# Kernel tuning notes

Hardware: AMD Instinct MI355X
Metric: run time of the kernel (lower is better)

## Reference

```python
import jax, jax.numpy as jnp
import numpy as np

FP8_E4M3_MAX = 448.0
AMAX_EPS = 1e-12


def _mlp(x, W1, b1, W2, b2):
    # wrapped sub-module: standard FFN block, exact (erf) GELU like nn.GELU
    h = jax.nn.gelu(x @ W1 + b1, approximate=False)  # [B,S,F]
    return h @ W2 + b2                               # [B,S,D]


def _quantize(t):
    # FP8ActivationStorage.quantize, simulated (int16) path:
    # amax -> scale = 448/amax -> scale*clamp -> cast int16 (truncates toward zero)
    amax = jnp.maximum(jnp.max(jnp.abs(t)), AMAX_EPS)
    scale = (FP8_E4M3_MAX / amax).astype(jnp.float32)
    q = jnp.clip(t.astype(jnp.float32) * scale, -FP8_E4M3_MAX, FP8_E4M3_MAX).astype(jnp.int16)
    return q, scale


def setup_inputs() -> dict:
    key = jax.random.key(0)
    k0, k1, k2 = jax.random.split(key, 3)
    B, S, D, F = 4, 4096, 2048, 8192
    x = jax.random.normal(k0, (B, S, D), dtype=jnp.float32)
    W1 = jax.random.normal(k1, (D, F), dtype=jnp.float32) * (1.0 / np.sqrt(D))
    b1 = jnp.zeros((F,), dtype=jnp.float32)
    W2 = jax.random.normal(k2, (F, D), dtype=jnp.float32) * (1.0 / np.sqrt(F))
    b2 = jnp.zeros((D,), dtype=jnp.float32)
    return {"x": x, "W1": W1, "b1": b1, "W2": W2, "b2": b2}


def reference(x, W1, b1, W2, b2):
    # Forward of _FP8CheckpointWrapper: run module on the ORIGINAL input,
    # and also compute the quantized copy that would be saved for backward.
    out = _mlp(x, W1, b1, W2, b2)
    q, scale = _quantize(jax.lax.stop_gradient(x))
    return out, q, scale
```

## Files before the change

### kernel.cpp

```cpp
#include <hip/hip_runtime.h>
#include <hip/hip_bf16.h>
#include <stdint.h>

#define BS_M 16384
#define DD   2048
#define FF   8192

typedef __attribute__((ext_vector_type(8))) short bf16x8;
typedef __attribute__((ext_vector_type(4))) float f32x4;

__device__ __forceinline__ void load_lds16(const void* g, void* l) {
  __builtin_amdgcn_global_load_lds(
      (const __attribute__((address_space(1))) uint32_t*)g,
      (__attribute__((address_space(3))) uint32_t*)l,
      16, 0, 0);
}

__device__ __forceinline__ ushort f2bf(float v) {
  __hip_bfloat16 b = __float2bfloat16(v);
  return *reinterpret_cast<ushort*>(&b);
}

#define SBAR() asm volatile("s_barrier" ::: "memory")
#define VMCNT(n)                                             \
  do {                                                       \
    asm volatile("s_waitcnt vmcnt(" #n ")" ::: "memory");    \
    __builtin_amdgcn_sched_barrier(0);                       \
  } while (0)

__global__ void amax_kernel(const float4* __restrict__ x, int n4,
                            unsigned* __restrict__ amax) {
  float m = 0.f;
  const int stride = gridDim.x * blockDim.x;
  int i = blockIdx.x * blockDim.x + threadIdx.x;
  for (; i + 3 * stride < n4; i += 4 * stride) {
    float4 a = x[i];
    float4 b = x[i + stride];
    float4 c = x[i + 2 * stride];
    float4 d = x[i + 3 * stride];
    float ma = fmaxf(fmaxf(fabsf(a.x), fabsf(a.y)), fmaxf(fabsf(a.z), fabsf(a.w)));
    float mb = fmaxf(fmaxf(fabsf(b.x), fabsf(b.y)), fmaxf(fabsf(b.z), fabsf(b.w)));
    float mc = fmaxf(fmaxf(fabsf(c.x), fabsf(c.y)), fmaxf(fabsf(c.z), fabsf(c.w)));
    float md = fmaxf(fmaxf(fabsf(d.x), fabsf(d.y)), fmaxf(fabsf(d.z), fabsf(d.w)));
    m = fmaxf(m, fmaxf(fmaxf(ma, mb), fmaxf(mc, md)));
  }
  for (; i < n4; i += stride) {
    float4 a = x[i];
    m = fmaxf(m, fmaxf(fmaxf(fabsf(a.x), fabsf(a.y)),
                       fmaxf(fabsf(a.z), fabsf(a.w))));
  }
#pragma unroll
  for (int o = 32; o; o >>= 1) m = fmaxf(m, __shfl_xor(m, o));
  __shared__ float wm[4];
  if ((threadIdx.x & 63) == 0) wm[threadIdx.x >> 6] = m;
  __syncthreads();
  if (threadIdx.x == 0) {
    m = fmaxf(fmaxf(wm[0], wm[1]), fmaxf(wm[2], wm[3]));
    atomicMax(amax, __float_as_uint(m));
  }
}

__global__ void quant_cvt(const float4* __restrict__ x, ushort* __restrict__ xbf,
                          float4* __restrict__ q, float* __restrict__ scale_out,
                          const unsigned* __restrict__ amax_bits, int n4) {
  const float amax = fmaxf(__uint_as_float(*amax_bits), 1e-12f);
  const float scale = 448.0f / amax;
  if (blockIdx.x == 0 && threadIdx.x == 0) *scale_out = scale;
  const int stride = gridDim.x * blockDim.x;
  int i = blockIdx.x * blockDim.x + threadIdx.x;
  for (; i + 3 * stride < n4; i += 4 * stride) {
    float4 v[4];
    v[0] = x[i]; v[1] = x[i + stride]; v[2] = x[i + 2 * stride]; v[3] = x[i + 3 * stride];
#pragma unroll
    for (int u = 0; u < 4; ++u) {
      int idx = i + u * stride;
      ushort4 b;
      b.x = f2bf(v[u].x); b.y = f2bf(v[u].y); b.z = f2bf(v[u].z); b.w = f2bf(v[u].w);
      *(ushort4*)&xbf[(size_t)idx * 4] = b;
      float4 qq;
      qq.x = truncf(fminf(fmaxf(v[u].x * scale, -448.f), 448.f));
      qq.y = truncf(fminf(fmaxf(v[u].y * scale, -448.f), 448.f));
      qq.z = truncf(fminf(fmaxf(v[u].z * scale, -448.f), 448.f));
      qq.w = truncf(fminf(fmaxf(v[u].w * scale, -448.f), 448.f));
      q[idx] = qq;
    }
  }
  for (; i < n4; i += stride) {
    float4 v = x[i];
    ushort4 b;
    b.x = f2bf(v.x); b.y = f2bf(v.y); b.z = f2bf(v.z); b.w = f2bf(v.w);
    *(ushort4*)&xbf[(size_t)i * 4] = b;
    float4 qq;
    qq.x = truncf(fminf(fmaxf(v.x * scale, -448.f), 448.f));
    qq.y = truncf(fminf(fmaxf(v.y * scale, -448.f), 448.f));
    qq.z = truncf(fminf(fmaxf(v.z * scale, -448.f), 448.f));
    qq.w = truncf(fminf(fmaxf(v.w * scale, -448.f), 448.f));
    q[i] = qq;
  }
}

__global__ void transpose_cvt(const float* __restrict__ in,
                              ushort* __restrict__ out, int R, int C) {
  __shared__ float tile[32][33];
  const int tx = threadIdx.x, ty = threadIdx.y;
  const int c0 = blockIdx.x << 5, r0 = blockIdx.y << 5;
#pragma unroll
  for (int i = 0; i < 32; i += 8)
    tile[ty + i][tx] = in[(size_t)(r0 + ty + i) * C + c0 + tx];
  __syncthreads();
#pragma unroll
  for (int i = 0; i < 32; i += 8)
    out[(size_t)(c0 + ty + i) * R + r0 + tx] = f2bf(tile[tx][ty + i]);
}

template <int FUSE>
__global__ __launch_bounds__(512, 1) void gemm8p(
    const ushort* __restrict__ A, const ushort* __restrict__ Bt,
    const float* __restrict__ bias, void* __restrict__ Cv,
    int M, int N, int K) {
  __shared__ ushort lds[8 * 8192];

  const int tiles_n = N >> 8;
  const int nwg = gridDim.x;
  const int q8 = nwg >> 3;
  const int b = blockIdx.x;
  const int swz = (b & 7) * q8 + (b >> 3);
  const int brow = (swz / tiles_n) << 8;
  const int bcol = (swz % tiles_n) << 8;

  const int tid = threadIdx.x;
  const int wave = tid >> 6, lane = tid & 63;
  const int wr = wave >> 2, wc = wave & 3;
  const int fr = lane & 15, kg = lane >> 4;

  const int srow = tid >> 2;
  const int g2e = (((tid & 3) ^ ((tid >> 3) & 3)) << 3);
  const size_t aoff0 = (size_t)(brow + srow) * K;
  const size_t aoff1 = (size_t)(brow + 128 + srow) * K;
  const size_t boff0 = (size_t)(bcol + srow) * K;
  const size_t boff1 = (size_t)(bcol + 128 + srow) * K;

  const int rkey = ((fr >> 1) & 3) << 4;
  const int gsel = (((kg << 4) ^ rkey)) >> 1;
  const int abase = (wr * 128 + fr) * 32 + gsel;
  const int bbase = (wc * 64 + fr) * 32 + gsel;

#define U(c, mat, kh) (lds + (((c) * 4 + (mat) * 2 + (kh)) << 13))
#define STAGE_A(u, kcol)                                       \
  do {                                                         \
    load_lds16(A + aoff0 + (kcol) + g2e, (u) + wave * 512);    \
    load_lds16(A + aoff1 + (kcol) + g2e, (u) + 4096 + wave * 512); \
  } while (0)
#define STAGE_B(u, kcol)                                       \
  do {                                                         \
    load_lds16(Bt + boff0 + (kcol) + g2e, (u) + wave * 512);   \
    load_lds16(Bt + boff1 + (kcol) + g2e, (u) + 4096 + wave * 512); \
  } while (0)
#define RD_A(u)                                                \
  {                                                            \
    _Pragma("unroll") for (int m = 0; m < 8; ++m)              \
        aF[m] = *(const bf16x8*)((u) + abase + m * 512);       \
  }
#define RD_B01(u)                                              \
  {                                                            \
    bF[0] = *(const bf16x8*)((u) + bbase);                     \
    bF[1] = *(const bf16x8*)((u) + bbase + 512);               \
  }
#define RD_B23(u)                                              \
  {                                                            \
    bF[2] = *(const bf16x8*)((u) + bbase + 1024);              \
    bF[3] = *(const bf16x8*)((u) + bbase + 1536);              \
  }
#define MM(n0)                                                             \
  {                                                                        \
    __builtin_amdgcn_s_setprio(1);                                         \
    _Pragma("unroll") for (int m = 0; m < 8; ++m) {                        \
      acc[m][n0] = __builtin_amdgcn_mfma_f32_16x16x32_bf16(                \
          aF[m], bF[n0], acc[m][n0], 0, 0, 0);                             \
      acc[m][(n0) + 1] = __builtin_amdgcn_mfma_f32_16x16x32_bf16(          \
          aF[m], bF[(n0) + 1], acc[m][(n0) + 1], 0, 0, 0);                 \
    }                                                                      \
    __builtin_amdgcn_s_setprio(0);                                         \
  }

  f32x4 acc[8][4] = {};
  bf16x8 aF[8];
  bf16x8 bF[4];

  const int NT = K >> 6;

  STAGE_A(U(0, 0, 0), 0);
  STAGE_B(U(0, 1, 0), 0);
  STAGE_A(U(0, 0, 1), 32);
  STAGE_B(U(0, 1, 1), 32);
  VMCNT(4);
  SBAR();

  for (int t = 0; t < NT - 1; ++t) {
    const int c = t & 1;
    const int kn = (t + 1) << 6;
    ushort* uA0 = U(c, 0, 0);
    ushort* uB0 = U(c, 1, 0);
    ushort* uA1 = U(c, 0, 1);
    ushort* uB1 = U(c, 1, 1);
    RD_A(uA0);
    RD_B01(uB0);
    STAGE_A(U(c ^ 1, 0, 0), kn);
    SBAR();
    MM(0);
    SBAR();
    RD_B23(uB0);
    STAGE_B(U(c ^ 1, 1, 0), kn);
    SBAR();
    MM(2);
    VMCNT(4);
    SBAR();
    RD_A(uA1);
    RD_B01(uB1);
    STAGE_A(U(c ^ 1, 0, 1), kn + 32);
    SBAR();
    MM(0);
    SBAR();
    RD_B23(uB1);
    STAGE_B(U(c ^ 1, 1, 1), kn + 32);
    SBAR();
    MM(2);
    VMCNT(4);
    SBAR();
  }

  {
    const int c = (NT - 1) & 1;
    RD_A(U(c, 0, 0));
    RD_B01(U(c, 1, 0));
    SBAR();
    MM(0);
    SBAR();
    RD_B23(U(c, 1, 0));
    SBAR();
    MM(2);
    VMCNT(0);
    SBAR();
    RD_A(U(c, 0, 1));
    RD_B01(U(c, 1, 1));
    SBAR();
    MM(0);
    SBAR();
    RD_B23(U(c, 1, 1));
    MM(2);
  }

  float bv[4];
#pragma unroll
  for (int n = 0; n < 4; ++n) bv[n] = bias[bcol + wc * 64 + n * 16 + fr];
#pragma unroll
  for (int m = 0; m < 8; ++m) {
    const int r0 = brow + wr * 128 + m * 16 + kg * 4;
#pragma unroll
    for (int n = 0; n < 4; ++n) {
      const int col = bcol + wc * 64 + n * 16 + fr;
#pragma unroll
      for (int r = 0; r < 4; ++r) {
        float v = acc[m][n][r] + bv[n];
        if (FUSE) {
          v = 0.5f * v * (1.0f + erff(v * 0.70710678118f));
          ((ushort*)Cv)[(size_t)(r0 + r) * N + col] = f2bf(v);
        } else {
          ((float*)Cv)[(size_t)(r0 + r) * N + col] = v;
        }
      }
    }
  }
#undef U
#undef STAGE_A
#undef STAGE_B
#undef RD_A
#undef RD_B01
#undef RD_B23
#undef MM
}

extern "C" void kernel_launch(void* const* d_in, const int* in_sizes, int n_in,
                              void* d_out, int out_size, void* d_ws,
                              size_t ws_size, hipStream_t stream) {
  const float* x  = (const float*)d_in[0];
  const float* W1 = (const float*)d_in[1];
  const float* b1 = (const float*)d_in[2];
  const float* W2 = (const float*)d_in[3];
  const float* b2 = (const float*)d_in[4];

  const size_t MD = (size_t)BS_M * DD;
  const size_t MF = (size_t)BS_M * FF;
  const size_t DF = (size_t)DD * FF;

  float* out_mlp = (float*)d_out;
  float* q_out   = out_mlp + MD;
  float* s_out   = out_mlp + 2 * MD;

  ushort* xbf = (ushort*)d_ws;
  ushort* w1t = xbf + MD;
  ushort* w2t = w1t + DF;
  ushort* hbf = w2t + DF;
  unsigned* amax = (unsigned*)(hbf + MF);

  hipMemsetAsync(amax, 0, sizeof(unsigned), stream);

  const int n4 = (int)(MD / 4);
  amax_kernel<<<2048, 256, 0, stream>>>((const float4*)x, n4, amax);
  quant_cvt<<<2048, 256, 0, stream>>>((const float4*)x, xbf, (float4*)q_out,
                                      s_out, amax, n4);
  transpose_cvt<<<dim3(FF / 32, DD / 32), dim3(32, 8), 0, stream>>>(W1, w1t, DD, FF);
  transpose_cvt<<<dim3(DD / 32, FF / 32), dim3(32, 8), 0, stream>>>(W2, w2t, FF, DD);
  gemm8p<1><<<(BS_M / 256) * (FF / 256), 512, 0, stream>>>(xbf, w1t, b1, hbf,
                                                           BS_M, FF, DD);
  gemm8p<0><<<(BS_M / 256) * (DD / 256), 512, 0, stream>>>(hbf, w2t, b2,
                                                           out_mlp, BS_M, DD, FF);
}
```

Before: 1.536 ms.

## Double-buffer register fragments to overlap LDS reads with MFMA in GEMM loop

Adds a second set of A and B register fragments so the LDS reads for the next half-tile are issued before the MFMA block that consumes the current fragments. Each MFMA phase is moved one step ahead of its reads, and the vmcnt waits are tightened to 2. The aim is to hide LDS read latency behind matrix math. In exchange, VGPR pressure rises (an extra 8+4 bf16x8 fragments), which could reduce occupancy or cause spills.

```diff
diff --git a/kernel.cpp b/kernel.cpp
--- a/kernel.cpp
+++ b/kernel.cpp
@@ -146,46 +146,37 @@
   const int bbase = (wc * 64 + fr) * 32 + gsel;
 
 #define U(c, mat, kh) (lds + (((c) * 4 + (mat) * 2 + (kh)) << 13))
-#define STAGE_A(u, kcol)                                       \
-  do {                                                         \
-    load_lds16(A + aoff0 + (kcol) + g2e, (u) + wave * 512);    \
+#define STAGE_A(u, kcol)                                           \
+  do {                                                             \
+    load_lds16(A + aoff0 + (kcol) + g2e, (u) + wave * 512);        \
     load_lds16(A + aoff1 + (kcol) + g2e, (u) + 4096 + wave * 512); \
   } while (0)
-#define STAGE_B(u, kcol)                                       \
-  do {                                                         \
-    load_lds16(Bt + boff0 + (kcol) + g2e, (u) + wave * 512);   \
-    load_lds16(Bt + boff1 + (kcol) + g2e, (u) + 4096 + wave * 512); \
+#define STAGE_B(u, kcol)                                           \
+  do {                                                             \
+    load_lds16(Bt + boff0 + (kcol) + g2e, (u) + wave * 512);       \
+    load_lds16(Bt + boff1 + (kcol) + g2e, (u) + 4096 + wave * 512);\
   } while (0)
-#define RD_A(u)                                                \
-  {                                                            \
-    _Pragma("unroll") for (int m = 0; m < 8; ++m)              \
-        aF[m] = *(const bf16x8*)((u) + abase + m * 512);       \
-  }
-#define RD_B01(u)                                              \
-  {                                                            \
-    bF[0] = *(const bf16x8*)((u) + bbase);                     \
-    bF[1] = *(const bf16x8*)((u) + bbase + 512);               \
-  }
-#define RD_B23(u)                                              \
-  {                                                            \
-    bF[2] = *(const bf16x8*)((u) + bbase + 1024);              \
-    bF[3] = *(const bf16x8*)((u) + bbase + 1536);              \
-  }
-#define MM(n0)                                                             \
+#define RD_A8(dst, u)                                              \
+  {                                                                \
+    _Pragma("unroll") for (int m = 0; m < 8; ++m)                  \
+        dst[m] = *(const bf16x8*)((u) + abase + m * 512);          \
+  }
+#define RDB(u, n) (*(const bf16x8*)((u) + bbase + (n) * 512))
+#define MM2(AF, b0v, b1v, n0, n1)                                          \
   {                                                                        \
     __builtin_amdgcn_s_setprio(1);                                         \
     _Pragma("unroll") for (int m = 0; m < 8; ++m) {                        \
       acc[m][n0] = __builtin_amdgcn_mfma_f32_16x16x32_bf16(                \
-          aF[m], bF[n0], acc[m][n0], 0, 0, 0);                             \
-      acc[m][(n0) + 1] = __builtin_amdgcn_mfma_f32_16x16x32_bf16(          \
-          aF[m], bF[(n0) + 1], acc[m][(n0) + 1], 0, 0, 0);                 \
+          AF[m], (b0v), acc[m][n0], 0, 0, 0);                              \
+      acc[m][n1] = __builtin_amdgcn_mfma_f32_16x16x32_bf16(                \
+          AF[m], (b1v), acc[m][n1], 0, 0, 0);                              \
     }                                                                      \
     __builtin_amdgcn_s_setprio(0);                                         \
   }
 
   f32x4 acc[8][4] = {};
-  bf16x8 aF[8];
-  bf16x8 bF[4];
+  bf16x8 aF0[8], aF1[8];
+  bf16x8 bA[4], bB[4];
 
   const int NT = K >> 6;
 
@@ -195,59 +186,71 @@
   STAGE_B(U(0, 1, 1), 32);
   VMCNT(4);
   SBAR();
+  RD_A8(aF0, U(0, 0, 0));
+  bA[0] = RDB(U(0, 1, 0), 0);
+  bA[1] = RDB(U(0, 1, 0), 1);
 
   for (int t = 0; t < NT - 1; ++t) {
     const int c = t & 1;
     const int kn = (t + 1) << 6;
-    ushort* uA0 = U(c, 0, 0);
     ushort* uB0 = U(c, 1, 0);
     ushort* uA1 = U(c, 0, 1);
     ushort* uB1 = U(c, 1, 1);
-    RD_A(uA0);
-    RD_B01(uB0);
-    STAGE_A(U(c ^ 1, 0, 0), kn);
-    SBAR();
-    MM(0);
-    SBAR();
-    RD_B23(uB0);
-    STAGE_B(U(c ^ 1, 1, 0), kn);
-    SBAR();
-    MM(2);
-    VMCNT(4);
-    SBAR();
-    RD_A(uA1);
-    RD_B01(uB1);
+    ushort* nA0 = U(c ^ 1, 0, 0);
+    ushort* nB0 = U(c ^ 1, 1, 0);
+    bA[2] = RDB(uB0, 2);
+    bA[3] = RDB(uB0, 3);
+    STAGE_A(nA0, kn);
+    SBAR();
+    MM2(aF0, bA[0], bA[1], 0, 1);
+    VMCNT(2);
+    SBAR();
+    RD_A8(aF1, uA1);
+    bB[0] = RDB(uB1, 0);
+    bB[1] = RDB(uB1, 1);
+    STAGE_B(nB0, kn);
+    SBAR();
+    MM2(aF0, bA[2], bA[3], 2, 3);
+    SBAR();
+    bB[2] = RDB(uB1, 2);
+    bB[3] = RDB(uB1, 3);
     STAGE_A(U(c ^ 1, 0, 1), kn + 32);
     SBAR();
-    MM(0);
-    SBAR();
-    RD_B23(uB1);
+    MM2(aF1, bB[0], bB[1], 0, 1);
+    VMCNT(2);
+    SBAR();
+    RD_A8(aF0, nA0);
+    bA[0] = RDB(nB0, 0);
+    bA[1] = RDB(nB0, 1);
     STAGE_B(U(c ^ 1, 1, 1), kn + 32);
     SBAR();
-    MM(2);
-    VMCNT(4);
+    MM2(aF1, bB[2], bB[3], 2, 3);
     SBAR();
   }
 
   {
     const int c = (NT - 1) & 1;
-    RD_A(U(c, 0, 0));
-    RD_B01(U(c, 1, 0));
-    SBAR();
-    MM(0);
-    SBAR();
-    RD_B23(U(c, 1, 0));
-    SBAR();
-    MM(2);
+    ushort* uB0 = U(c, 1, 0);
+    ushort* uA1 = U(c, 0, 1);
+    ushort* uB1 = U(c, 1, 1);
+    bA[2] = RDB(uB0, 2);
+    bA[3] = RDB(uB0, 3);
+    SBAR();
+    MM2(aF0, bA[0], bA[1], 0, 1);
     VMCNT(0);
     SBAR();
-    RD_A(U(c, 0, 1));
-    RD_B01(U(c, 1, 1));
-    SBAR();
-    MM(0);
-    SBAR();
-    RD_B23(U(c, 1, 1));
-    MM(2);
+    RD_A8(aF1, uA1);
+    bB[0] = RDB(uB1, 0);
+    bB[1] = RDB(uB1, 1);
+    SBAR();
+    MM2(aF0, bA[2], bA[3], 2, 3);
+    SBAR();
+    bB[2] = RDB(uB1, 2);
+    bB[3] = RDB(uB1, 3);
+    SBAR();
+    MM2(aF1, bB[0], bB[1], 0, 1);
+    SBAR();
+    MM2(aF1, bB[2], bB[3], 2, 3);
   }
 
   float bv[4];
@@ -274,10 +277,9 @@
 #undef U
 #undef STAGE_A
 #undef STAGE_B
-#undef RD_A
-#undef RD_B01
-#undef RD_B23
-#undef MM
+#undef RD_A8
+#undef RDB
+#undef MM2
 }
 
 extern "C" void kernel_launch(void* const* d_in, const int* in_sizes, int n_in,
```

After: 1.611 ms. 4.8% more time.
